# Kernel optimization log

Measured on AMD Instinct MI355X. Metric: run time of the kernel, lower is better.

Reference implementation:

```python
import jax, jax.numpy as jnp
import numpy as np

B, S, D, H = 2, 2048, 2048, 16
HD = D // H  # 128


def apply_rotary(xq, xk, cos, sin):
    # xq, xk: [B, S, H, HD]; cos, sin: [S, HD//2]
    def rot(x):
        xr = x.astype(jnp.float32).reshape(*x.shape[:-1], -1, 2)  # [B,S,H,HD/2,2]
        xe, xo = xr[..., 0], xr[..., 1]
        c = cos[None, :, None, :]
        s = sin[None, :, None, :]
        out_e = xe * c - xo * s
        out_o = xe * s + xo * c
        out = jnp.stack([out_e, out_o], axis=-1).reshape(x.shape)
        return out.astype(x.dtype)
    return rot(xq), rot(xk)


def setup_inputs() -> dict:
    key = jax.random.key(0)
    ks = jax.random.split(key, 8)
    x = jax.random.normal(ks[0], (B, S, D), dtype=jnp.float32)
    scale = 1.0 / np.sqrt(D)
    wq = jax.random.normal(ks[1], (D, D), dtype=jnp.float32) * scale
    wk = jax.random.normal(ks[2], (D, D), dtype=jnp.float32) * scale
    wv = jax.random.normal(ks[3], (D, D), dtype=jnp.float32) * scale
    wo = jax.random.normal(ks[4], (D, D), dtype=jnp.float32) * scale
    # RoPE frequencies (standard LLaMA): theta = 10000
    inv_freq = 1.0 / (10000.0 ** (np.arange(0, HD, 2, dtype=np.float32) / HD))
    t = np.arange(S, dtype=np.float32)
    ang = np.outer(t, inv_freq)  # [S, HD/2]
    freqs_cos = jnp.asarray(np.cos(ang))
    freqs_sin = jnp.asarray(np.sin(ang))
    # causal additive mask [1,1,S,S]
    neg = jnp.full((S, S), -1e9, dtype=jnp.float32)
    mask = jnp.triu(neg, k=1)[None, None, :, :]
    return {"x": x, "start_pos": 0, "freqs_cos": freqs_cos, "freqs_sin": freqs_sin,
            "mask": mask, "wq": wq, "wk": wk, "wv": wv, "wo": wo}


def reference(x, start_pos, freqs_cos, freqs_sin, mask, wq, wk, wv, wo):
    bsz, seqlen, dim = x.shape
    xq = (x @ wq.T).reshape(bsz, seqlen, H, HD)
    xk = (x @ wk.T).reshape(bsz, seqlen, H, HD)
    xv = (x @ wv.T).reshape(bsz, seqlen, H, HD)
    xq, xk = apply_rotary(xq, xk, freqs_cos, freqs_sin)
    # [B,H,S,HD]
    q = xq.transpose(0, 2, 1, 3)
    k = xk.transpose(0, 2, 1, 3)
    v = xv.transpose(0, 2, 1, 3)
    scores = jnp.einsum('bhqd,bhkd->bhqk', q, k) / jnp.sqrt(jnp.float32(HD))
    scores = scores + mask
    probs = jax.nn.softmax(scores.astype(jnp.float32), axis=-1).astype(q.dtype)
    out = jnp.einsum('bhqk,bhkd->bhqd', probs, v)
    out = out.transpose(0, 2, 1, 3).reshape(bsz, seqlen, dim)
    return out @ wo.T
```

## Files before the change

kernel.cpp:

```cpp
#include <hip/hip_runtime.h>
#include <cstdint>

typedef unsigned short u16;
typedef __attribute__((ext_vector_type(8))) short bf16x8;
typedef __attribute__((ext_vector_type(4))) float f32x4;

#define S_LEN 2048
#define DM    2048
#define NH    16
#define HDIM  128

__device__ __forceinline__ u16 f2bf(float f) {
  union { float f; unsigned u; } v; v.f = f;
  unsigned r = v.u + 0x7fffu + ((v.u >> 16) & 1u);
  return (u16)(r >> 16);
}
__device__ __forceinline__ float bf2f(u16 h) {
  union { unsigned u; float f; } v; v.u = ((unsigned)h) << 16;
  return v.f;
}

typedef __attribute__((address_space(3))) void lds_void_t;
typedef const __attribute__((address_space(1))) void gbl_void_t;
__device__ __forceinline__ void gload_lds16(const void* g, void* l) {
  __builtin_amdgcn_global_load_lds((gbl_void_t*)g, (lds_void_t*)l, 16, 0, 0);
}

#define VMCNTN(nn) asm volatile("s_waitcnt vmcnt(%0)" :: "n"(nn) : "memory")
#define LGKMCNT0() asm volatile("s_waitcnt lgkmcnt(0)" ::: "memory")

__global__ void cvt5_k(const float* s0, u16* d0, int n0,
                       const float* s1, u16* d1, int n1,
                       const float* s2, u16* d2, int n2,
                       const float* s3, u16* d3, int n3,
                       const float* s4, u16* d4, int n4) {
  const int stride = gridDim.x * blockDim.x;
  const int tid = blockIdx.x * blockDim.x + threadIdx.x;
#define CVT(S, D, N)                                        \
  for (int i = tid; i < ((N) >> 2); i += stride) {          \
    float4 v = ((const float4*)(S))[i];                     \
    ushort4 o;                                              \
    o.x = f2bf(v.x); o.y = f2bf(v.y);                       \
    o.z = f2bf(v.z); o.w = f2bf(v.w);                       \
    ((ushort4*)(D))[i] = o;                                 \
  }
  CVT(s0, d0, n0) CVT(s1, d1, n1) CVT(s2, d2, n2)
  CVT(s3, d3, n3) CVT(s4, d4, n4)
#undef CVT
}

template <int BM, int BN, int M, int N, int K, typename CT, int MODE>
__global__ __launch_bounds__(512, 2) void gemm8(const u16* __restrict__ A,
                                                const u16* __restrict__ Bm,
                                                CT* __restrict__ C,
                                                const float* __restrict__ fc,
                                                const float* __restrict__ fs,
                                                u16* __restrict__ qtp,
                                                u16* __restrict__ ktp) {
  constexpr int PWM = BM / 2, PWN = BN / 4;
  constexpr int MR = PWM / 16, NR = PWN / 16;
  constexpr int LA = BM / 128, LB = BN / 128;
  constexpr int VMK = LA + LB;
  constexpr int LDSA = BM * 32, LDSB = BN * 32;
  constexpr int nbn = N / BN, nbm = M / BM;
  constexpr int nwg = nbm * nbn;
  constexpr int GM = 8;
  __shared__ u16 sA[2 * LDSA];
  __shared__ u16 sB[2 * LDSB];

  const int t = threadIdx.x;
  const int lane = t & 63, wid = t >> 6;
  const int r0 = lane & 15, kq = lane >> 4;
  const int wr = wid >> 2, wc = wid & 3;

  const int bid = blockIdx.x;
  const int wgl = (bid & 7) * (nwg >> 3) + (bid >> 3);
  const int gid = wgl / (GM * nbn);
  const int rem = wgl % (GM * nbn);
  const long tile_m = (long)(gid * GM + (rem & (GM - 1))) * BM;
  const long tile_n = (long)(rem >> 3) * BN;

  constexpr int NPH = K / 32;

  const int swzcol = ((t & 3) ^ ((t >> 3) & 3)) * 8;
  const u16* gA = A + (tile_m + (t >> 2)) * (long)K + swzcol;
  const u16* gB = Bm + (tile_n + (t >> 2)) * (long)K + swzcol;

  auto stage = [&](int h) {
    u16* ba = &sA[(h & 1) * LDSA] + wid * 512;
    u16* bb = &sB[(h & 1) * LDSB] + wid * 512;
    const long coff = (long)h * 32;
#pragma unroll
    for (int r = 0; r < LA; ++r)
      gload_lds16(gA + (long)(r * 128) * K + coff, ba + r * 4096);
#pragma unroll
    for (int r = 0; r < LB; ++r)
      gload_lds16(gB + (long)(r * 128) * K + coff, bb + r * 4096);
  };

  const int rdslot = (kq ^ ((r0 >> 1) & 3)) * 8;
  const int aoff = (wr * PWM + r0) * 32 + rdslot;
  const int boff = (wc * PWN + r0) * 32 + rdslot;

  f32x4 acc[MR][NR];
#pragma unroll
  for (int m = 0; m < MR; ++m)
#pragma unroll
    for (int n = 0; n < NR; ++n) acc[m][n] = (f32x4){0.f, 0.f, 0.f, 0.f};

  stage(0); stage(1);
  VMCNTN(VMK);
  __builtin_amdgcn_s_barrier();

  for (int h = 0; h < NPH; ++h) {
    const u16* ra = &sA[(h & 1) * LDSA] + aoff;
    const u16* rb = &sB[(h & 1) * LDSB] + boff;
    bf16x8 a[MR], b[NR];
#pragma unroll
    for (int m = 0; m < MR; ++m) a[m] = *(const bf16x8*)(ra + m * 512);
#pragma unroll
    for (int n = 0; n < NR; ++n) b[n] = *(const bf16x8*)(rb + n * 512);
    LGKMCNT0();
    __builtin_amdgcn_s_barrier();
    stage(h + 2);
    __builtin_amdgcn_s_setprio(1);
#pragma unroll
    for (int m = 0; m < MR; ++m)
#pragma unroll
      for (int n = 0; n < NR; ++n)
        acc[m][n] = __builtin_amdgcn_mfma_f32_16x16x32_bf16(a[m], b[n],
                                                            acc[m][n], 0, 0, 0);
    __builtin_amdgcn_s_setprio(0);
    VMCNTN(VMK);
    __builtin_amdgcn_s_barrier();
  }

  if constexpr (MODE == 1) {
    const int z = (int)(tile_n >> 11);
    if (z == 2) {
#pragma unroll
      for (int m = 0; m < MR; ++m)
#pragma unroll
        for (int n = 0; n < NR; ++n)
#pragma unroll
          for (int r = 0; r < 4; ++r) {
            long grow = tile_m + wr * PWM + m * 16 + kq * 4 + r;
            long gcol = tile_n + wc * PWN + n * 16 + r0;
            C[grow * N + gcol] = (CT)f2bf(acc[m][n][r]);
          }
    } else {
      const float qsc = 0.12751743202f;
#pragma unroll
      for (int m = 0; m < MR; ++m)
#pragma unroll
        for (int n = 0; n < NR; ++n)
#pragma unroll
          for (int r = 0; r < 4; ++r) {
            long grow = tile_m + wr * PWM + m * 16 + kq * 4 + r;
            long gcol = tile_n + wc * PWN + n * 16 + r0;
            int srow = (int)(grow & 2047), bidx = (int)(grow >> 11);
            int h = ((int)gcol >> 7) & 15, hd = (int)gcol & 127;
            float v = acc[m][n][r];
            float partner = __shfl_xor(v, 1);
            int hd2 = hd >> 1;
            float c = fc[srow * 64 + hd2], sn = fs[srow * 64 + hd2];
            float res = (r0 & 1) ? (partner * sn + v * c)
                                 : (v * c - partner * sn);
            if (z == 0) res *= qsc;
            u16* dst = z ? ktp : qtp;
            dst[((long)(bidx * 16 + h) * S_LEN + srow) * HDIM + hd] = f2bf(res);
          }
    }
  } else {
#pragma unroll
    for (int m = 0; m < MR; ++m)
#pragma unroll
      for (int n = 0; n < NR; ++n)
#pragma unroll
        for (int r = 0; r < 4; ++r) {
          long grow = tile_m + wr * PWM + m * 16 + kq * 4 + r;
          long gcol = tile_n + wc * PWN + n * 16 + r0;
          float v = acc[m][n][r];
          if constexpr (sizeof(CT) == 2) C[grow * N + gcol] = (CT)f2bf(v);
          else                           C[grow * N + gcol] = v;
        }
  }
}

__global__ void vtrans_k(const u16* __restrict__ qkv, u16* __restrict__ vt) {
  __shared__ u16 tile[64][65];
  int bh = blockIdx.z;
  int b = bh >> 4, h = bh & 15;
  int s0 = blockIdx.x * 64, d0 = blockIdx.y * 64;
  int tx = threadIdx.x, ty = threadIdx.y;
#pragma unroll
  for (int i = 0; i < 64; i += 4) {
    int s = s0 + ty + i;
    tile[ty + i][tx] = qkv[((long)(b * S_LEN + s)) * 6144 + 4096 + h * HDIM + d0 + tx];
  }
  __syncthreads();
#pragma unroll
  for (int i = 0; i < 64; i += 4) {
    int d = d0 + ty + i;
    vt[((long)bh * HDIM + d) * S_LEN + s0 + tx] = tile[tx][ty + i];
  }
}

__global__ __launch_bounds__(128) void flash_k(const u16* __restrict__ qt,
                                               const u16* __restrict__ kt,
                                               const u16* __restrict__ vt,
                                               u16* __restrict__ attn) {
  constexpr int PS = 40;
  __shared__ u16 pbuf[2][2][32 * PS];
  const int t = threadIdx.x, lane = t & 63, wid = t >> 6;
  const int r0 = lane & 15, kq = lane >> 4;
  const int bh = blockIdx.x, b = bh >> 4, h = bh & 15;
  const int tile = (gridDim.y - 1) - blockIdx.y;
  const int q0w = tile * 64 + wid * 32;
  const int crow = kq * 4;

  const u16* qb = qt + ((long)bh * S_LEN + q0w) * HDIM;
  const u16* kb = kt + (long)bh * S_LEN * HDIM;
  const u16* vb = vt + (long)bh * HDIM * S_LEN;
  u16* pb0 = &pbuf[0][wid][0];
  u16* pb1 = &pbuf[1][wid][0];

  bf16x8 aq[2][4];
#pragma unroll
  for (int qc = 0; qc < 2; ++qc)
#pragma unroll
    for (int kk = 0; kk < 4; ++kk)
      aq[qc][kk] = *(const bf16x8*)(qb + (qc * 16 + r0) * HDIM + kk * 32 + kq * 8);

  f32x4 o[2][8];
  float mrow[2] = {-1e30f, -1e30f}, lrow[2] = {0.f, 0.f};
#pragma unroll
  for (int qc = 0; qc < 2; ++qc)
#pragma unroll
    for (int dt = 0; dt < 8; ++dt) o[qc][dt] = (f32x4){0.f, 0.f, 0.f, 0.f};

  bf16x8 bkA[2][4], bkB[2][4], bvA[8], bvB[8];
  f32x4 saccA[2][2], saccB[2][2];

  auto loadK = [&](bf16x8 (&dst)[2][4], int kv) {
#pragma unroll
    for (int kc = 0; kc < 2; ++kc)
#pragma unroll
      for (int kk = 0; kk < 4; ++kk)
        dst[kc][kk] = *(const bf16x8*)(kb + (long)(kv + kc * 16 + r0) * HDIM + kk * 32 + kq * 8);
  };
  auto loadV = [&](bf16x8 (&dst)[8], int kv) {
#pragma unroll
    for (int dt = 0; dt < 8; ++dt)
      dst[dt] = *(const bf16x8*)(vb + (long)(dt * 16 + r0) * S_LEN + kv + kq * 8);
  };
  auto qk = [&](bf16x8 (&kf)[2][4], f32x4 (&sacc)[2][2]) {
    __builtin_amdgcn_s_setprio(1);
#pragma unroll
    for (int kc = 0; kc < 2; ++kc) {
      f32x4 a0 = (f32x4){0.f, 0.f, 0.f, 0.f};
      f32x4 a1 = (f32x4){0.f, 0.f, 0.f, 0.f};
#pragma unroll
      for (int kk = 0; kk < 4; ++kk) {
        a0 = __builtin_amdgcn_mfma_f32_16x16x32_bf16(kf[kc][kk], aq[0][kk], a0, 0, 0, 0);
        a1 = __builtin_amdgcn_mfma_f32_16x16x32_bf16(kf[kc][kk], aq[1][kk], a1, 0, 0, 0);
      }
      sacc[kc][0] = a0; sacc[kc][1] = a1;
    }
    __builtin_amdgcn_s_setprio(0);
  };
  auto softmax_store = [&](f32x4 (&sacc)[2][2], int kv0, u16* pb) {
    const bool diag = (kv0 == q0w);
#pragma unroll
    for (int qc = 0; qc < 2; ++qc) {
      float s[2][4];
#pragma unroll
      for (int kc = 0; kc < 2; ++kc)
#pragma unroll
        for (int r = 0; r < 4; ++r) {
          float v = sacc[kc][qc][r];
          if (diag && (kc * 16 + crow + r > qc * 16 + r0)) v = -1e30f;
          s[kc][r] = v;
        }
      float pm = fmaxf(fmaxf(fmaxf(s[0][0], s[0][1]), fmaxf(s[0][2], s[0][3])),
                       fmaxf(fmaxf(s[1][0], s[1][1]), fmaxf(s[1][2], s[1][3])));
      pm = fmaxf(pm, __shfl_xor(pm, 16));
      pm = fmaxf(pm, __shfl_xor(pm, 32));
      if (!__all(pm - mrow[qc] <= 11.5416f)) {
        float mnew = fmaxf(mrow[qc], pm);
        float co = exp2f(mrow[qc] - mnew);
        mrow[qc] = mnew;
        lrow[qc] *= co;
        float cod[4];
#pragma unroll
        for (int r = 0; r < 4; ++r)
          cod[r] = __shfl(co, (lane & 48) | (crow + r));
#pragma unroll
        for (int dt = 0; dt < 8; ++dt)
#pragma unroll
          for (int r = 0; r < 4; ++r)
            o[qc][dt][r] *= cod[r];
      }
      float p[2][4];
      float rs = 0.f;
#pragma unroll
      for (int kc = 0; kc < 2; ++kc)
#pragma unroll
        for (int r = 0; r < 4; ++r) {
          p[kc][r] = exp2f(s[kc][r] - mrow[qc]);
          rs += p[kc][r];
        }
      rs += __shfl_xor(rs, 16);
      rs += __shfl_xor(rs, 32);
      lrow[qc] += rs;
#pragma unroll
      for (int kc = 0; kc < 2; ++kc) {
        unsigned w0, w1;
        asm("v_cvt_pk_bf16_f32 %0, %1, %2" : "=v"(w0) : "v"(p[kc][0]), "v"(p[kc][1]));
        asm("v_cvt_pk_bf16_f32 %0, %1, %2" : "=v"(w1) : "v"(p[kc][2]), "v"(p[kc][3]));
        uint2 w; w.x = w0; w.y = w1;
        *(uint2*)(pb + (qc * 16 + r0) * PS + kc * 16 + crow) = w;
      }
    }
  };
  auto pv = [&](const u16* pb, bf16x8 (&bv)[8]) {
    bf16x8 pa0 = *(const bf16x8*)(pb + r0 * PS + kq * 8);
    bf16x8 pa1 = *(const bf16x8*)(pb + (16 + r0) * PS + kq * 8);
    __builtin_amdgcn_s_setprio(1);
#pragma unroll
    for (int dt = 0; dt < 8; ++dt) {
      o[0][dt] = __builtin_amdgcn_mfma_f32_16x16x32_bf16(pa0, bv[dt], o[0][dt], 0, 0, 0);
      o[1][dt] = __builtin_amdgcn_mfma_f32_16x16x32_bf16(pa1, bv[dt], o[1][dt], 0, 0, 0);
    }
    __builtin_amdgcn_s_setprio(0);
  };

  loadK(bkA, 0);
  if (32 <= q0w) loadK(bkB, 32);
  qk(bkA, saccA);
  int kv0 = 0;
  for (;;) {
    {
      const bool more = (kv0 + 32 <= q0w);
      loadV(bvA, kv0);
      softmax_store(saccA, kv0, pb0);
      if (more) qk(bkB, saccB);
      if (kv0 + 64 <= q0w) loadK(bkA, kv0 + 64);
      pv(pb0, bvA);
      kv0 += 32;
      if (!more) break;
    }
    {
      const bool more = (kv0 + 32 <= q0w);
      loadV(bvB, kv0);
      softmax_store(saccB, kv0, pb1);
      if (more) qk(bkA, saccA);
      if (kv0 + 64 <= q0w) loadK(bkB, kv0 + 64);
      pv(pb1, bvB);
      kv0 += 32;
      if (!more) break;
    }
  }

#pragma unroll
  for (int qc = 0; qc < 2; ++qc) {
    float linv[4];
#pragma unroll
    for (int r = 0; r < 4; ++r)
      linv[r] = 1.0f / __shfl(lrow[qc], (lane & 48) | (crow + r));
#pragma unroll
    for (int dt = 0; dt < 8; ++dt)
#pragma unroll
      for (int r = 0; r < 4; ++r) {
        int srow = q0w + qc * 16 + crow + r;
        attn[((long)(b * S_LEN + srow)) * DM + h * HDIM + dt * 16 + r0] =
            f2bf(o[qc][dt][r] * linv[r]);
      }
  }
}

extern "C" void kernel_launch(void* const* d_in, const int* in_sizes, int n_in,
                              void* d_out, int out_size, void* d_ws, size_t ws_size,
                              hipStream_t stream) {
  (void)in_sizes; (void)n_in; (void)out_size; (void)ws_size;
  const float* x  = (const float*)d_in[0];
  const float* fc = (const float*)d_in[2];
  const float* fs = (const float*)d_in[3];
  const float* wq = (const float*)d_in[5];
  const float* wk = (const float*)d_in[6];
  const float* wv = (const float*)d_in[7];
  const float* wo = (const float*)d_in[8];
  float* out = (float*)d_out;

  u16* xb   = (u16*)d_ws;
  u16* wqkv = xb + 8388608;
  u16* wob  = wqkv + 12582912;
  u16* qkv  = wob + 4194304;
  u16* qt   = qkv + 25165824;
  u16* kt   = qt + 8388608;
  u16* vt   = kt + 8388608;
  u16* attn = qkv;

  cvt5_k<<<2048, 256, 0, stream>>>(x, xb, 8388608,
                                   wq, wqkv, 4194304,
                                   wk, wqkv + 4194304, 4194304,
                                   wv, wqkv + 8388608, 4194304,
                                   wo, wob, 4194304);

  gemm8<128, 256, 4096, 6144, 2048, u16, 1><<<768, 512, 0, stream>>>(
      xb, wqkv, qkv, fc, fs, qt, kt);

  vtrans_k<<<dim3(32, 2, 32), dim3(64, 4), 0, stream>>>(qkv, vt);

  flash_k<<<dim3(32, 32), 128, 0, stream>>>(qt, kt, vt, attn);

  gemm8<128, 256, 4096, 2048, 2048, float, 0><<<256, 512, 0, stream>>>(
      attn, wob, out, nullptr, nullptr, nullptr, nullptr);
}
```

Before: 319.0 us.

## Fuse V transpose into QKV GEMM epilogue and prefetch V one step ahead

The QKV GEMM epilogue for V tiles now stages the bf16 accumulators transposed in LDS (reusing the operand buffers) and writes V directly in [b,h,d,s] layout. This removes the separate vtrans kernel and its extra global read and write of V. The flash kernel also loads V for the next KV block one iteration early, using the double-buffered registers, so the V load latency is hidden behind softmax and QK. In exchange, the GEMM epilogue gains an LDS round trip and extra barriers, and the flash kernel may use more registers.

```diff
diff --git a/kernel.cpp b/kernel.cpp
--- a/kernel.cpp
+++ b/kernel.cpp
@@ -56,17 +56,21 @@
                                                 const float* __restrict__ fc,
                                                 const float* __restrict__ fs,
                                                 u16* __restrict__ qtp,
-                                                u16* __restrict__ ktp) {
+                                                u16* __restrict__ ktp,
+                                                u16* __restrict__ vtp) {
   constexpr int PWM = BM / 2, PWN = BN / 4;
   constexpr int MR = PWM / 16, NR = PWN / 16;
   constexpr int LA = BM / 128, LB = BN / 128;
   constexpr int VMK = LA + LB;
   constexpr int LDSA = BM * 32, LDSB = BN * 32;
+  constexpr int STG = 2 * (LDSA + LDSB);
+  constexpr int SMEMSZ = (MODE == 1) ? (STG > BN * 132 ? STG : BN * 132) : STG;
   constexpr int nbn = N / BN, nbm = M / BM;
   constexpr int nwg = nbm * nbn;
   constexpr int GM = 8;
-  __shared__ u16 sA[2 * LDSA];
-  __shared__ u16 sB[2 * LDSB];
+  __shared__ u16 smem[SMEMSZ];
+  u16* sA = smem;
+  u16* sB = smem + 2 * LDSA;
 
   const int t = threadIdx.x;
   const int lane = t & 63, wid = t >> 6;
@@ -138,16 +142,30 @@
   if constexpr (MODE == 1) {
     const int z = (int)(tile_n >> 11);
     if (z == 2) {
+      VMCNTN(0);
+      __builtin_amdgcn_s_barrier();
+      u16* tb = smem;
 #pragma unroll
       for (int m = 0; m < MR; ++m)
 #pragma unroll
-        for (int n = 0; n < NR; ++n)
-#pragma unroll
-          for (int r = 0; r < 4; ++r) {
-            long grow = tile_m + wr * PWM + m * 16 + kq * 4 + r;
-            long gcol = tile_n + wc * PWN + n * 16 + r0;
-            C[grow * N + gcol] = (CT)f2bf(acc[m][n][r]);
-          }
+        for (int n = 0; n < NR; ++n) {
+          int row0 = wr * PWM + m * 16 + kq * 4;
+          int col  = wc * PWN + n * 16 + r0;
+          ushort4 pk;
+          pk.x = f2bf(acc[m][n][0]); pk.y = f2bf(acc[m][n][1]);
+          pk.z = f2bf(acc[m][n][2]); pk.w = f2bf(acc[m][n][3]);
+          *(ushort4*)(tb + col * 132 + row0) = pk;
+        }
+      __builtin_amdgcn_s_barrier();
+      const int bidx = (int)(tile_m >> 11), s0 = (int)(tile_m & 2047);
+#pragma unroll 4
+      for (int it2 = 0; it2 < 32; ++it2) {
+        int col = it2 * 8 + wid;
+        long gc = tile_n + col;
+        int h2 = ((int)gc >> 7) & 15, hd2 = (int)gc & 127;
+        unsigned vv = *(const unsigned*)(tb + col * 132 + 2 * lane);
+        *(unsigned*)(vtp + ((long)(bidx * 16 + h2) * HDIM + hd2) * S_LEN + s0 + 2 * lane) = vv;
+      }
     } else {
       const float qsc = 0.12751743202f;
 #pragma unroll
@@ -187,25 +205,6 @@
   }
 }
 
-__global__ void vtrans_k(const u16* __restrict__ qkv, u16* __restrict__ vt) {
-  __shared__ u16 tile[64][65];
-  int bh = blockIdx.z;
-  int b = bh >> 4, h = bh & 15;
-  int s0 = blockIdx.x * 64, d0 = blockIdx.y * 64;
-  int tx = threadIdx.x, ty = threadIdx.y;
-#pragma unroll
-  for (int i = 0; i < 64; i += 4) {
-    int s = s0 + ty + i;
-    tile[ty + i][tx] = qkv[((long)(b * S_LEN + s)) * 6144 + 4096 + h * HDIM + d0 + tx];
-  }
-  __syncthreads();
-#pragma unroll
-  for (int i = 0; i < 64; i += 4) {
-    int d = d0 + ty + i;
-    vt[((long)bh * HDIM + d) * S_LEN + s0 + tx] = tile[tx][ty + i];
-  }
-}
-
 __global__ __launch_bounds__(128) void flash_k(const u16* __restrict__ qt,
                                                const u16* __restrict__ kt,
                                                const u16* __restrict__ vt,
@@ -337,12 +336,13 @@
 
   loadK(bkA, 0);
   if (32 <= q0w) loadK(bkB, 32);
+  loadV(bvA, 0);
   qk(bkA, saccA);
   int kv0 = 0;
   for (;;) {
     {
       const bool more = (kv0 + 32 <= q0w);
-      loadV(bvA, kv0);
+      if (more) loadV(bvB, kv0 + 32);
       softmax_store(saccA, kv0, pb0);
       if (more) qk(bkB, saccB);
       if (kv0 + 64 <= q0w) loadK(bkA, kv0 + 64);
@@ -352,7 +352,7 @@
     }
     {
       const bool more = (kv0 + 32 <= q0w);
-      loadV(bvB, kv0);
+      if (more) loadV(bvA, kv0 + 32);
       softmax_store(saccB, kv0, pb1);
       if (more) qk(bkA, saccA);
       if (kv0 + 64 <= q0w) loadK(bkB, kv0 + 64);
@@ -408,12 +408,10 @@
                                    wo, wob, 4194304);
 
   gemm8<128, 256, 4096, 6144, 2048, u16, 1><<<768, 512, 0, stream>>>(
-      xb, wqkv, qkv, fc, fs, qt, kt);
-
-  vtrans_k<<<dim3(32, 2, 32), dim3(64, 4), 0, stream>>>(qkv, vt);
+      xb, wqkv, qkv, fc, fs, qt, kt, vt);
 
   flash_k<<<dim3(32, 32), 128, 0, stream>>>(qt, kt, vt, attn);
 
   gemm8<128, 256, 4096, 2048, 2048, float, 0><<<256, 512, 0, stream>>>(
-      attn, wob, out, nullptr, nullptr, nullptr, nullptr);
-}
+      attn, wob, out, nullptr, nullptr, nullptr, nullptr, nullptr);
+}
```

Result: faster. 292.7 us (-8.3%).
